# Kernel tuning notes

Measured on AMD Instinct MI355X. Metric: run time of the kernel, lower is better.

## Reference

```python
import jax, jax.numpy as jnp
import numpy as np

B, D, N, M = 64, 128, 400, 50
H, KD = 8, 16
NCONV, K, PAD = 4, 7, 3
MAXTS = 10000.0


def _pe(l):
    # PositionEncoding: freqs/phases interleave sin/cos as sin(pos*f + phase)
    i = np.arange(D)
    freqs = MAXTS ** np.where(i % 2 == 0, -i / D, -(i - 1) / D)
    phases = np.where(i % 2 == 0, 0.0, np.pi / 2)
    pos = np.arange(l)
    return jnp.asarray(np.sin(pos[None, :] * freqs[:, None] + phases[:, None]).astype(np.float32))  # [D, l]


def _ln(x, g, b, eps=1e-6):
    # LayerNorm1d over channel dim of [B, D, L]; torch .std() is unbiased (ddof=1), divides by (std+eps)
    mu = x.mean(axis=1, keepdims=True)
    sd = x.std(axis=1, keepdims=True, ddof=1)
    return g[None, :, None] * (x - mu) / (sd + eps) + b[None, :, None]


def _attn(xT, mask, Wq, bq, Wk, bk, Wv, bv, Wo, bo):
    # xT: [B, L, D]; per-head linears vectorized over the head axis
    q = jnp.einsum('bld,hdk->bhlk', xT, Wq) + bq[None, :, None, :]
    k = jnp.einsum('bld,hdk->bhlk', xT, Wk) + bk[None, :, None, :]
    v = jnp.einsum('bld,hdk->bhlk', xT, Wv) + bv[None, :, None, :]
    sc = jnp.einsum('bhik,bhjk->bhij', q, k) / np.sqrt(KD)
    sc = sc - 1e30 * (1.0 - mask[:, None, None, :])  # mask over key positions
    a = jax.nn.softmax(sc, axis=-1)
    o = jnp.einsum('bhij,bhjk->bhik', a, v)
    o = o.transpose(0, 2, 1, 3).reshape(xT.shape[0], xT.shape[1], H * KD)
    return o @ Wo + bo


def _fwd(context_emb, question_emb, c_mask, q_mask, ln_g, ln_b, dw_w, dw_b, pw_w, pw_b,
         Wq, bq, Wk, bk, Wv, bv, Wo, bo, Wfc, bfc, cq_wc, cq_wq, cq_wm, cq_b):
    def block(x, mask):
        out = x + _pe(x.shape[2])[None]
        for i in range(NCONV):  # fixed small layer loop
            res = out
            h = _ln(out, ln_g, ln_b)
            h = jax.lax.conv_general_dilated(h, dw_w[i], (1,), [(PAD, PAD)],
                                             feature_group_count=D,
                                             dimension_numbers=('NCH', 'OIH', 'NCH')) + dw_b[i][None, :, None]
            h = jnp.einsum('bdl,ed->bel', h, pw_w[i]) + pw_b[i][None, :, None]
            out = jax.nn.relu(h) + res  # eval-mode layer_dropout = inputs + residual
        res = out
        h = _ln(out, ln_g, ln_b)
        h = _attn(h.transpose(0, 2, 1), mask, Wq, bq, Wk, bk, Wv, bv, Wo, bo)
        out = h.transpose(0, 2, 1) + res
        res = out
        h = _ln(out, ln_g, ln_b)
        h = jnp.einsum('bdl,ed->bel', h, Wfc) + bfc[None, :, None]
        return h + res

    C = block(context_emb, c_mask)
    Q = block(question_emb, q_mask)
    C2 = C.transpose(0, 2, 1)  # [B, N, D]
    Q2 = Q.transpose(0, 2, 1)  # [B, M, D]
    # Biaffine similarity W0([Q; C; Q*C]) decomposed (same math, no [B,N*M,3D] materialization)
    S = (C2 @ cq_wc)[:, :, None] + (Q2 @ cq_wq)[:, None, :] \
        + jnp.einsum('bnd,bmd->bnm', C2 * cq_wm, Q2) + cq_b[0]
    S_r = jax.nn.softmax(S - 1e30 * (1.0 - q_mask[:, None, :]), axis=2)
    S_c = jax.nn.softmax(S - 1e30 * (1.0 - c_mask[:, :, None]), axis=1)
    A = S_r @ Q2                                    # context-to-query [B, N, D]
    Bt = jnp.einsum('bnm,bkm->bnk', S_r, S_c) @ C2  # query-to-context (DCN style) [B, N, D]
    return jnp.concatenate([C2, A, C2 * A, C2 * Bt], axis=-1)  # [B, N, 4D]


def setup_inputs() -> dict:
    key = jax.random.key(0)
    ks = jax.random.split(key, 16)
    s = 1.0 / np.sqrt(D)
    return dict(
        context_emb=jax.random.normal(ks[0], (B, D, N), jnp.float32),
        question_emb=jax.random.normal(ks[1], (B, D, M), jnp.float32),
        c_mask=jnp.ones((B, N), jnp.float32),
        q_mask=jnp.ones((B, M), jnp.float32),
        ln_g=jnp.ones((D,), jnp.float32),
        ln_b=jnp.zeros((D,), jnp.float32),
        dw_w=jax.random.normal(ks[2], (NCONV, D, 1, K), jnp.float32) / np.sqrt(K),
        dw_b=jnp.zeros((NCONV, D), jnp.float32),
        pw_w=jax.random.normal(ks[3], (NCONV, D, D), jnp.float32) * s,
        pw_b=jnp.zeros((NCONV, D), jnp.float32),
        Wq=jax.random.normal(ks[4], (H, D, KD), jnp.float32) * s,
        bq=jnp.zeros((H, KD), jnp.float32),
        Wk=jax.random.normal(ks[5], (H, D, KD), jnp.float32) * s,
        bk=jnp.zeros((H, KD), jnp.float32),
        Wv=jax.random.normal(ks[6], (H, D, KD), jnp.float32) * s,
        bv=jnp.zeros((H, KD), jnp.float32),
        Wo=jax.random.normal(ks[7], (H * KD, D), jnp.float32) * s,
        bo=jnp.zeros((D,), jnp.float32),
        Wfc=jax.random.normal(ks[8], (D, D), jnp.float32) * s,
        bfc=jnp.zeros((D,), jnp.float32),
        cq_wc=jax.random.normal(ks[9], (D,), jnp.float32) * s,
        cq_wq=jax.random.normal(ks[10], (D,), jnp.float32) * s,
        cq_wm=jax.random.normal(ks[11], (D,), jnp.float32) * s,
        cq_b=jnp.zeros((1,), jnp.float32),
    )


def reference(context_emb, question_emb, c_mask, q_mask, ln_g, ln_b, dw_w, dw_b, pw_w, pw_b,
              Wq, bq, Wk, bk, Wv, bv, Wo, bo, Wfc, bfc, cq_wc, cq_wq, cq_wm, cq_b):
    return _fwd(context_emb, question_emb, c_mask, q_mask, ln_g, ln_b, dw_w, dw_b, pw_w, pw_b,
                Wq, bq, Wk, bk, Wv, bv, Wo, bo, Wfc, bfc, cq_wc, cq_wq, cq_wm, cq_b)
```

## Files before the change

kernel.cpp:

```cpp
#include <hip/hip_runtime.h>
#include <math.h>

#define BB 64
#define DD 128
#define NN 400
#define MM 50
#define HH 8
#define KDIM 16
#define NC 4
#define KW 7

#define SZ_C (BB * DD * NN)
#define SZ_Q (BB * DD * MM)
#define SSTAT (BB * NN + BB * MM)

__global__ void k_transposeW(const float* __restrict__ pw_w, const float* __restrict__ Wo,
                             const float* __restrict__ Wfc, const float* __restrict__ Wq,
                             const float* __restrict__ Wk, const float* __restrict__ Wv,
                             float* __restrict__ Wcan) {
  int idx = blockIdx.x * 256 + threadIdx.x;
  if (idx >= 9 * 16384) return;
  int m = idx >> 14;
  int r = idx & 16383;
  int d = r >> 7, e = r & 127;
  float v;
  if (m < 4) v = pw_w[m * 16384 + e * 128 + d];
  else if (m == 4) v = Wo[d * 128 + e];
  else if (m == 5) v = Wfc[e * 128 + d];
  else {
    const float* W = (m == 6) ? Wq : (m == 7) ? Wk : Wv;
    v = W[((e >> 4) * 128 + d) * 16 + (e & 15)];
  }
  Wcan[idx] = v;
}

__global__ void k_pestats(const float* __restrict__ xC, const float* __restrict__ xQ,
                          float* __restrict__ yC, float* __restrict__ yQ,
                          float* __restrict__ mu, float* __restrict__ inv) {
  int blk = blockIdx.x;
  const float* x; float* y; int L, l0, b, soff;
  if (blk < 448) { b = blk / 7; l0 = (blk % 7) * 64; x = xC; y = yC; L = NN; soff = 0; }
  else { b = blk - 448; l0 = 0; x = xQ; y = yQ; L = MM; soff = BB * NN; }
  int tid = threadIdx.x;
  int ll = tid & 63;
  int dq = tid >> 6;
  int l = l0 + ll;
  __shared__ float s_sum[4][64], s_sq[4][64];
  float sum = 0.f, sq = 0.f;
  if (l < L) {
    const float* px = x + (size_t)b * DD * L + l;
    float* py = y + (size_t)b * DD * L + l;
    for (int d = dq * 32; d < dq * 32 + 32; ++d) {
      int de = d & ~1;
      float freq = __expf((float)de * (-9.210340371976184f / 128.0f));
      float ph = (d & 1) ? 1.5707963267948966f : 0.0f;
      float v = px[(size_t)d * L] + sinf((float)l * freq + ph);
      py[(size_t)d * L] = v;
      sum += v; sq += v * v;
    }
  }
  s_sum[dq][ll] = sum; s_sq[dq][ll] = sq;
  __syncthreads();
  if (dq == 0 && l < L) {
    float ts = s_sum[0][ll] + s_sum[1][ll] + s_sum[2][ll] + s_sum[3][ll];
    float tq = s_sq[0][ll] + s_sq[1][ll] + s_sq[2][ll] + s_sq[3][ll];
    float m = ts * (1.0f / 128.0f);
    float var = (tq - 128.0f * m * m) * (1.0f / 127.0f);
    float sd = sqrtf(fmaxf(var, 0.f));
    mu[soff + b * L + l] = m;
    inv[soff + b * L + l] = 1.0f / (sd + 1e-6f);
  }
}

__global__ __launch_bounds__(256, 2) void k_convgemm(
    const float* __restrict__ xC, const float* __restrict__ xQ,
    float* __restrict__ outC, float* __restrict__ outQ,
    const float* __restrict__ Wc, const float* __restrict__ pwb,
    const float* __restrict__ dww, const float* __restrict__ dwb,
    const float* __restrict__ muI, const float* __restrict__ invI,
    float* __restrict__ muO, float* __restrict__ invO,
    const float* __restrict__ g, const float* __restrict__ beta) {
  int blk = blockIdx.x;
  int b = blk >> 3, tile = blk & 7;
  const float* x; float* out; int L, l0, soff;
  if (tile < 7) { x = xC; out = outC; L = NN; l0 = tile * 64; soff = 0; }
  else { x = xQ; out = outQ; L = MM; l0 = 0; soff = BB * NN; }
  __shared__ float Wl[32 * 128];
  __shared__ float Xl[32 * 64];
  __shared__ float Sm[70], Si[70];
  int tid = threadIdx.x;
  const float* xb = x + (size_t)b * DD * L;
  for (int t = tid; t < 70; t += 256) {
    int gl = l0 + t - 3;
    bool ok = (gl >= 0 && gl < L);
    Sm[t] = ok ? muI[soff + b * L + gl] : 0.f;
    Si[t] = ok ? invI[soff + b * L + gl] : 0.f;
  }
  float acc[8][4];
  #pragma unroll
  for (int i = 0; i < 8; ++i)
    #pragma unroll
    for (int j = 0; j < 4; ++j) acc[i][j] = 0.f;
  __syncthreads();
  for (int kc = 0; kc < 4; ++kc) {
    int d0 = kc * 32;
    #pragma unroll
    for (int i = 0; i < 4; ++i) {
      int idx = i * 256 + tid;
      ((float4*)Wl)[idx] = ((const float4*)Wc)[(size_t)d0 * 32 + idx];
    }
    #pragma unroll
    for (int r = 0; r < 2; ++r) {
      int k = r * 16 + (tid >> 4);
      int d = d0 + k;
      int c0 = (tid & 15) * 4;
      const float* xrow = xb + (size_t)d * L;
      float gd = g[d], bd = beta[d];
      float wv[7];
      #pragma unroll
      for (int u = 0; u < 7; ++u) wv[u] = dww[d * 7 + u];
      float dbv = dwb[d];
      float xw[10];
      int gbase = l0 + c0 - 3;
      if (gbase >= 1 && gbase + 11 <= L && (((unsigned)(d * L + gbase - 1)) & 3u) == 0u) {
        const float4* p = (const float4*)&xrow[gbase - 1];
        float4 A = p[0], Bv = p[1], Cv = p[2];
        float xr[12] = {A.x, A.y, A.z, A.w, Bv.x, Bv.y, Bv.z, Bv.w, Cv.x, Cv.y, Cv.z, Cv.w};
        #pragma unroll
        for (int s = 0; s < 10; ++s)
          xw[s] = gd * (xr[s + 1] - Sm[c0 + s]) * Si[c0 + s] + bd;
      } else {
        #pragma unroll
        for (int s = 0; s < 10; ++s) {
          int gl = gbase + s;
          float v = 0.f;
          if (gl >= 0 && gl < L)
            v = gd * (xrow[gl] - Sm[c0 + s]) * Si[c0 + s] + bd;
          xw[s] = v;
        }
      }
      float4 o;
      o.x = dbv; o.y = dbv; o.z = dbv; o.w = dbv;
      #pragma unroll
      for (int u = 0; u < 7; ++u) {
        o.x += wv[u] * xw[u];
        o.y += wv[u] * xw[u + 1];
        o.z += wv[u] * xw[u + 2];
        o.w += wv[u] * xw[u + 3];
      }
      *(float4*)&Xl[k * 64 + c0] = o;
    }
    __syncthreads();
    int e0 = (tid >> 4) * 8, cq = (tid & 15) * 4;
    for (int k = 0; k < 32; ++k) {
      const float4* wp = (const float4*)&Wl[k * 128 + e0];
      float4 w0 = wp[0], w1 = wp[1];
      float4 xv = *(const float4*)&Xl[k * 64 + cq];
      float we[8] = {w0.x, w0.y, w0.z, w0.w, w1.x, w1.y, w1.z, w1.w};
      float xe[4] = {xv.x, xv.y, xv.z, xv.w};
      #pragma unroll
      for (int i = 0; i < 8; ++i)
        #pragma unroll
        for (int j = 0; j < 4; ++j) acc[i][j] += we[i] * xe[j];
    }
    __syncthreads();
  }
  int e0 = (tid >> 4) * 8, cq = (tid & 15) * 4;
  float ssum[4], ssq[4];
  #pragma unroll
  for (int j = 0; j < 4; ++j) { ssum[j] = 0.f; ssq[j] = 0.f; }
  #pragma unroll
  for (int i = 0; i < 8; ++i) {
    float bi = pwb[e0 + i];
    float* po = out + ((size_t)b * DD + e0 + i) * L;
    const float* pr = xb + (size_t)(e0 + i) * L;
    #pragma unroll
    for (int j = 0; j < 4; ++j) {
      int l = l0 + cq + j;
      if (l < L) {
        float v = fmaxf(acc[i][j] + bi, 0.f) + pr[l];
        po[l] = v;
        ssum[j] += v; ssq[j] += v * v;
      }
    }
  }
  int grp = tid >> 4;
  #pragma unroll
  for (int j = 0; j < 4; ++j) {
    Xl[grp * 64 + cq + j] = ssum[j];
    Wl[grp * 64 + cq + j] = ssq[j];
  }
  __syncthreads();
  if (tid < 64) {
    int l = l0 + tid;
    if (l < L) {
      float ts = 0.f, tq = 0.f;
      #pragma unroll
      for (int gg = 0; gg < 16; ++gg) { ts += Xl[gg * 64 + tid]; tq += Wl[gg * 64 + tid]; }
      float m = ts * (1.0f / 128.0f);
      float var = (tq - 128.0f * m * m) * (1.0f / 127.0f);
      float sd = sqrtf(fmaxf(var, 0.f));
      muO[soff + b * L + l] = m;
      invO[soff + b * L + l] = 1.0f / (sd + 1e-6f);
    }
  }
}

template <int LNF, int ACT, int STATS, int TRANS>
__global__ __launch_bounds__(256) void k_gemm64(
    const float* __restrict__ xC, const float* __restrict__ xQ,
    float* __restrict__ outC, float* __restrict__ outQ,
    const float* __restrict__ Wc, const float* __restrict__ bias,
    const float* __restrict__ mu, const float* __restrict__ inv,
    float* __restrict__ muO, float* __restrict__ invO,
    const float* __restrict__ g, const float* __restrict__ beta,
    float* __restrict__ C2o, float* __restrict__ Q2o,
    float* __restrict__ cdo, float* __restrict__ qdo,
    const float* __restrict__ wc, const float* __restrict__ wq) {
  int blk = blockIdx.x;
  int b = blk >> 3, tile = blk & 7;
  const float* x; float* out; int L, l0, soff;
  if (tile < 7) { x = xC; out = outC; L = NN; l0 = tile * 64; soff = 0; }
  else { x = xQ; out = outQ; L = MM; l0 = 0; soff = BB * NN; }
  __shared__ float Wl[TRANS ? 64 * 68 : 32 * 128];
  __shared__ float Xl[TRANS ? 64 * 68 : 32 * 64];
  int tid = threadIdx.x;
  float acc[8][4];
  #pragma unroll
  for (int i = 0; i < 8; ++i)
    #pragma unroll
    for (int j = 0; j < 4; ++j) acc[i][j] = 0.f;
  const float* xb = x + (size_t)b * DD * L;
  const float* pmu = mu + soff + b * L;
  const float* pin = inv + soff + b * L;
  for (int kc = 0; kc < 4; ++kc) {
    int d0 = kc * 32;
    #pragma unroll
    for (int i = 0; i < 4; ++i) {
      int idx = i * 256 + tid;
      ((float4*)Wl)[idx] = ((const float4*)Wc)[(size_t)d0 * 32 + idx];
    }
    #pragma unroll
    for (int t = 0; t < 8; ++t) {
      int idx = t * 256 + tid;
      int k = idx >> 6, l = idx & 63;
      float v = 0.f;
      int gl = l0 + l;
      if (gl < L) {
        v = xb[(size_t)(d0 + k) * L + gl];
        if (LNF) v = g[d0 + k] * (v - pmu[gl]) * pin[gl] + beta[d0 + k];
      }
      Xl[idx] = v;
    }
    __syncthreads();
    int e0 = (tid >> 4) * 8, cq = (tid & 15) * 4;
    for (int k = 0; k < 32; ++k) {
      const float4* wp = (const float4*)&Wl[k * 128 + e0];
      float4 w0 = wp[0], w1 = wp[1];
      float4 xv = *(const float4*)&Xl[k * 64 + cq];
      float we[8] = {w0.x, w0.y, w0.z, w0.w, w1.x, w1.y, w1.z, w1.w};
      float xe[4] = {xv.x, xv.y, xv.z, xv.w};
      #pragma unroll
      for (int i = 0; i < 8; ++i)
        #pragma unroll
        for (int j = 0; j < 4; ++j) acc[i][j] += we[i] * xe[j];
    }
    __syncthreads();
  }
  int e0 = (tid >> 4) * 8, cq = (tid & 15) * 4;
  float ssum[4], ssq[4];
  #pragma unroll
  for (int j = 0; j < 4; ++j) { ssum[j] = 0.f; ssq[j] = 0.f; }
  #pragma unroll
  for (int i = 0; i < 8; ++i) {
    float bi = bias[e0 + i];
    float* po = out + ((size_t)b * DD + e0 + i) * L;
    #pragma unroll
    for (int j = 0; j < 4; ++j) {
      int l = l0 + cq + j;
      if (l < L) {
        float v = acc[i][j] + bi;
        if (ACT != 0) v += po[l];
        po[l] = v;
        if (STATS) { ssum[j] += v; ssq[j] += v * v; }
        if (TRANS) {
          float* T = (e0 < 64) ? Wl : Xl;
          T[(cq + j) * 68 + (e0 & 63) + i] = v;
        }
      }
    }
  }
  if (STATS) {
    int grp = tid >> 4;
    #pragma unroll
    for (int j = 0; j < 4; ++j) {
      Xl[grp * 64 + cq + j] = ssum[j];
      Wl[grp * 64 + cq + j] = ssq[j];
    }
    __syncthreads();
    if (tid < 64) {
      int l = l0 + tid;
      if (l < L) {
        float ts = 0.f, tq = 0.f;
        #pragma unroll
        for (int gg = 0; gg < 16; ++gg) { ts += Xl[gg * 64 + tid]; tq += Wl[gg * 64 + tid]; }
        float m = ts * (1.0f / 128.0f);
        float var = (tq - 128.0f * m * m) * (1.0f / 127.0f);
        float sd = sqrtf(fmaxf(var, 0.f));
        muO[soff + b * L + l] = m;
        invO[soff + b * L + l] = 1.0f / (sd + 1e-6f);
      }
    }
  }
  if (TRANS) {
    __syncthreads();
    int r = tid >> 2, seg = tid & 3;
    int gl = l0 + r;
    const float* wsel = (tile < 7) ? wc : wq;
    float* Y2 = (tile < 7) ? C2o : Q2o;
    float* dd = (tile < 7) ? cdo : qdo;
    float part = 0.f;
    if (gl < L) {
      float4* dst = (float4*)(Y2 + ((size_t)b * L + gl) * 128);
      #pragma unroll
      for (int q8 = 0; q8 < 8; ++q8) {
        int e = seg * 32 + q8 * 4;
        const float* T = (e < 64) ? Wl : Xl;
        float4 v4 = *(const float4*)&T[r * 68 + (e & 63)];
        dst[seg * 8 + q8] = v4;
        float4 w4 = *(const float4*)&wsel[e];
        part += v4.x * w4.x + v4.y * w4.y + v4.z * w4.z + v4.w * w4.w;
      }
    }
    part += __shfl_xor(part, 1);
    part += __shfl_xor(part, 2);
    if (gl < L && seg == 0) dd[b * L + gl] = part;
  }
}

__global__ __launch_bounds__(256) void k_gemm_qkv(
    const float* __restrict__ xC, const float* __restrict__ xQ,
    float* __restrict__ o1C, float* __restrict__ o1Q,
    float* __restrict__ o2C, float* __restrict__ o2Q,
    float* __restrict__ o3C, float* __restrict__ o3Q,
    const float* __restrict__ Wcan,
    const float* __restrict__ bq, const float* __restrict__ bk, const float* __restrict__ bv,
    const float* __restrict__ mu, const float* __restrict__ inv,
    const float* __restrict__ g, const float* __restrict__ beta) {
  int blk0 = blockIdx.x;
  int grp = blk0 >> 9;
  int blk = blk0 & 511;
  const float* Wc = Wcan + (size_t)(6 + grp) * 16384;
  const float* bias = (grp == 0) ? bq : (grp == 1) ? bk : bv;
  float* oC = (grp == 0) ? o1C : (grp == 1) ? o2C : o3C;
  float* oQ = (grp == 0) ? o1Q : (grp == 1) ? o2Q : o3Q;
  int b = blk >> 3, tile = blk & 7;
  const float* x; float* out; int L, l0, soff;
  if (tile < 7) { x = xC; out = oC; L = NN; l0 = tile * 64; soff = 0; }
  else { x = xQ; out = oQ; L = MM; l0 = 0; soff = BB * NN; }
  __shared__ float Wl[32 * 128];
  __shared__ float Xl[32 * 64];
  int tid = threadIdx.x;
  float acc[8][4];
  #pragma unroll
  for (int i = 0; i < 8; ++i)
    #pragma unroll
    for (int j = 0; j < 4; ++j) acc[i][j] = 0.f;
  const float* xb = x + (size_t)b * DD * L;
  const float* pmu = mu + soff + b * L;
  const float* pin = inv + soff + b * L;
  for (int kc = 0; kc < 4; ++kc) {
    int d0 = kc * 32;
    #pragma unroll
    for (int i = 0; i < 4; ++i) {
      int idx = i * 256 + tid;
      ((float4*)Wl)[idx] = ((const float4*)Wc)[(size_t)d0 * 32 + idx];
    }
    #pragma unroll
    for (int t = 0; t < 8; ++t) {
      int idx = t * 256 + tid;
      int k = idx >> 6, l = idx & 63;
      float v = 0.f;
      int gl = l0 + l;
      if (gl < L) {
        v = xb[(size_t)(d0 + k) * L + gl];
        v = g[d0 + k] * (v - pmu[gl]) * pin[gl] + beta[d0 + k];
      }
      Xl[idx] = v;
    }
    __syncthreads();
    int e0 = (tid >> 4) * 8, cq = (tid & 15) * 4;
    for (int k = 0; k < 32; ++k) {
      const float4* wp = (const float4*)&Wl[k * 128 + e0];
      float4 w0 = wp[0], w1 = wp[1];
      float4 xv = *(const float4*)&Xl[k * 64 + cq];
      float we[8] = {w0.x, w0.y, w0.z, w0.w, w1.x, w1.y, w1.z, w1.w};
      float xe[4] = {xv.x, xv.y, xv.z, xv.w};
      #pragma unroll
      for (int i = 0; i < 8; ++i)
        #pragma unroll
        for (int j = 0; j < 4; ++j) acc[i][j] += we[i] * xe[j];
    }
    __syncthreads();
  }
  int e0 = (tid >> 4) * 8, cq = (tid & 15) * 4;
  #pragma unroll
  for (int i = 0; i < 8; ++i) {
    float bi = bias[e0 + i];
    float* po = out + ((size_t)b * DD + e0 + i) * L;
    #pragma unroll
    for (int j = 0; j < 4; ++j) {
      int l = l0 + cq + j;
      if (l < L) po[l] = acc[i][j] + bi;
    }
  }
}

__global__ __launch_bounds__(256) void k_attn2(
    const float* __restrict__ qC, const float* __restrict__ kC, const float* __restrict__ vC,
    const float* __restrict__ qQ, const float* __restrict__ kQ, const float* __restrict__ vQ,
    const float* __restrict__ cmask, const float* __restrict__ qmask,
    float* __restrict__ oC, float* __restrict__ oQ) {
  int blk = blockIdx.x;
  const float *qp, *kp, *vp, *mk; float* op; int L, b, h, q0, qcnt;
  if (blk < 1024) {
    b = blk >> 4; h = (blk >> 1) & 7; int half = blk & 1;
    qp = qC; kp = kC; vp = vC; mk = cmask; op = oC; L = NN;
    q0 = half * 256; qcnt = half ? (NN - 256) : 256;
  } else {
    int bb = blk - 1024; b = bb >> 3; h = bb & 7;
    qp = qQ; kp = kQ; vp = vQ; mk = qmask; op = oQ; L = MM;
    q0 = 0; qcnt = MM;
  }
  __shared__ float Kl[NN * KDIM];
  __shared__ float Vl[NN * KDIM];
  __shared__ float Ml[NN];
  int tid = threadIdx.x;
  size_t base = ((size_t)b * DD + h * KDIM) * L;
  int KP = (L + 7) & ~7;
  for (int idx = tid; idx < KDIM * L; idx += 256) {
    int t = idx / L, j = idx - t * L;
    Kl[j * KDIM + t] = kp[base + (size_t)t * L + j];
    Vl[j * KDIM + t] = vp[base + (size_t)t * L + j];
  }
  for (int idx = tid; idx < (KP - L) * KDIM; idx += 256) {
    int j = L + (idx >> 4), t = idx & 15;
    Kl[j * KDIM + t] = 0.f; Vl[j * KDIM + t] = 0.f;
  }
  for (int j = tid; j < KP; j += 256)
    Ml[j] = (j < L) ? -1e30f * (1.0f - mk[b * L + j]) : -1e30f;
  __syncthreads();
  if (tid >= qcnt) return;

  int i = q0 + tid;
  float q[KDIM];
  #pragma unroll
  for (int t = 0; t < KDIM; ++t) q[t] = qp[base + (size_t)t * L + i] * 0.25f;
  float m = -1e30f, ls = 0.f;
  float acc[KDIM];
  #pragma unroll
  for (int t = 0; t < KDIM; ++t) acc[t] = 0.f;
  for (int j0 = 0; j0 < KP; j0 += 8) {
    const float4* mp = (const float4*)&Ml[j0];
    float4 ma0 = mp[0], ma1 = mp[1];
    float mav[8] = {ma0.x, ma0.y, ma0.z, ma0.w, ma1.x, ma1.y, ma1.z, ma1.w};
    float s[8];
    #pragma unroll
    for (int jj = 0; jj < 8; ++jj) {
      const float4* kf = (const float4*)&Kl[(j0 + jj) * KDIM];
      float4 k0 = kf[0], k1 = kf[1], k2 = kf[2], k3 = kf[3];
      float da = q[0] * k0.x + q[1] * k0.y + q[2] * k0.z + q[3] * k0.w
               + q[4] * k1.x + q[5] * k1.y + q[6] * k1.z + q[7] * k1.w;
      float db = q[8] * k2.x + q[9] * k2.y + q[10] * k2.z + q[11] * k2.w
               + q[12] * k3.x + q[13] * k3.y + q[14] * k3.z + q[15] * k3.w;
      s[jj] = da + db + mav[jj];
    }
    float cm = s[0];
    #pragma unroll
    for (int jj = 1; jj < 8; ++jj) cm = fmaxf(cm, s[jj]);
    if (cm > m) {
      float sc = __expf(m - cm);
      ls *= sc;
      #pragma unroll
      for (int t = 0; t < KDIM; ++t) acc[t] *= sc;
      m = cm;
    }
    #pragma unroll
    for (int jj = 0; jj < 8; ++jj) {
      float p = __expf(s[jj] - m);
      ls += p;
      const float4* vf = (const float4*)&Vl[(j0 + jj) * KDIM];
      float4 v0 = vf[0], v1 = vf[1], v2 = vf[2], v3 = vf[3];
      acc[0] += p * v0.x;  acc[1] += p * v0.y;  acc[2] += p * v0.z;  acc[3] += p * v0.w;
      acc[4] += p * v1.x;  acc[5] += p * v1.y;  acc[6] += p * v1.z;  acc[7] += p * v1.w;
      acc[8] += p * v2.x;  acc[9] += p * v2.y;  acc[10] += p * v2.z; acc[11] += p * v2.w;
      acc[12] += p * v3.x; acc[13] += p * v3.y; acc[14] += p * v3.z; acc[15] += p * v3.w;
    }
  }
  float invl = 1.0f / ls;
  #pragma unroll
  for (int t = 0; t < KDIM; ++t)
    op[base + (size_t)t * L + i] = acc[t] * invl;
}

__global__ __launch_bounds__(256) void k_S2(
    const float* __restrict__ C2, const float* __restrict__ Q2,
    const float* __restrict__ cd, const float* __restrict__ qd,
    const float* __restrict__ wm, const float* __restrict__ bias,
    float* __restrict__ S) {
  int blk = blockIdx.x;
  int b = blk / 7, nt = blk % 7;
  int n0 = nt * 64;
  int nv = NN - n0; if (nv > 64) nv = 64;
  __shared__ float Cw[64 * 132];
  __shared__ float Ql[52 * 132];
  __shared__ float cdl[64];
  __shared__ float qdl[50];
  int tid = threadIdx.x;
  const float4* c4g = (const float4*)(C2 + (size_t)b * NN * DD);
  const float4* q4g = (const float4*)(Q2 + (size_t)b * MM * DD);
  const float4* w4 = (const float4*)wm;
  for (int i = tid; i < 64 * 32; i += 256) {
    int n = i >> 5, d4 = i & 31;
    float4 v = {0.f, 0.f, 0.f, 0.f};
    if (n < nv) {
      float4 c = c4g[(size_t)(n0 + n) * 32 + d4];
      float4 w = w4[d4];
      v.x = c.x * w.x; v.y = c.y * w.y; v.z = c.z * w.z; v.w = c.w * w.w;
    }
    *(float4*)&Cw[n * 132 + d4 * 4] = v;
  }
  for (int i = tid; i < 52 * 32; i += 256) {
    int m = i >> 5, d4 = i & 31;
    float4 v = {0.f, 0.f, 0.f, 0.f};
    if (m < MM) v = q4g[(size_t)m * 32 + d4];
    *(float4*)&Ql[m * 132 + d4 * 4] = v;
  }
  if (tid < 64) cdl[tid] = (tid < nv) ? cd[b * NN + n0 + tid] : 0.f;
  if (tid >= 64 && tid < 114) qdl[tid - 64] = qd[b * MM + (tid - 64)];
  __syncthreads();
  int n = tid >> 2, mg = tid & 3;
  int m0 = mg * 13;
  float acc[13];
  #pragma unroll
  for (int k = 0; k < 13; ++k) acc[k] = 0.f;
  const float* cp = &Cw[n * 132];
  for (int d4 = 0; d4 < 32; ++d4) {
    float4 c = *(const float4*)&cp[d4 * 4];
    #pragma unroll
    for (int k = 0; k < 13; ++k) {
      float4 q = *(const float4*)&Ql[(m0 + k) * 132 + d4 * 4];
      acc[k] += c.x * q.x + c.y * q.y + c.z * q.z + c.w * q.w;
    }
  }
  if (n < nv) {
    float add = cdl[n] + bias[0];
    float* ps = S + ((size_t)b * NN + n0 + n) * MM + m0;
    #pragma unroll
    for (int k = 0; k < 13; ++k) {
      int m = m0 + k;
      if (m < MM) ps[k] = acc[k] + add + qdl[m];
    }
  }
}

__global__ void k_smaxU(const float* __restrict__ S, float* __restrict__ Sr,
                        const float* __restrict__ cmask, const float* __restrict__ qmask,
                        const float* __restrict__ C2, float* __restrict__ U) {
  int blk = blockIdx.x;
  int tid = threadIdx.x;
  if (blk < BB * MM) {
    int b = blk / MM;
    int mcol = blk % MM;
    __shared__ float Sl[NN];
    float vals[7];
    float mx = -1e30f;
    #pragma unroll
    for (int c = 0; c < 7; ++c) {
      int n = tid + c * 64;
      float s = -1e30f;
      if (n < NN)
        s = S[((size_t)b * NN + n) * MM + mcol] - 1e30f * (1.0f - cmask[b * NN + n]);
      vals[c] = s;
      mx = fmaxf(mx, s);
    }
    #pragma unroll
    for (int off = 1; off < 64; off <<= 1) mx = fmaxf(mx, __shfl_xor(mx, off));
    float sum = 0.f;
    #pragma unroll
    for (int c = 0; c < 7; ++c) { vals[c] = __expf(vals[c] - mx); sum += vals[c]; }
    #pragma unroll
    for (int off = 1; off < 64; off <<= 1) sum += __shfl_xor(sum, off);
    float inv = 1.0f / sum;
    #pragma unroll
    for (int c = 0; c < 7; ++c) {
      int n = tid + c * 64;
      if (n < NN) Sl[n] = vals[c] * inv;
    }
    __syncthreads();
    const float2* c2 = (const float2*)(C2 + (size_t)b * NN * DD) + tid;
    float2 a = {0.f, 0.f};
    #pragma unroll 4
    for (int kk = 0; kk < NN; ++kk) {
      float s = Sl[kk];
      float2 c = c2[(size_t)kk * 64];
      a.x += s * c.x; a.y += s * c.y;
    }
    ((float2*)(U + ((size_t)b * MM + mcol) * DD))[tid] = a;
  } else {
    int bn = blk - BB * MM;
    int b = bn / NN;
    float s = -1e30f;
    if (tid < MM)
      s = S[(size_t)bn * MM + tid] - 1e30f * (1.0f - qmask[b * MM + tid]);
    float mx = s;
    #pragma unroll
    for (int off = 1; off < 64; off <<= 1) mx = fmaxf(mx, __shfl_xor(mx, off));
    float e = (tid < MM) ? __expf(s - mx) : 0.f;
    float sum = e;
    #pragma unroll
    for (int off = 1; off < 64; off <<= 1) sum += __shfl_xor(sum, off);
    if (tid < MM) Sr[(size_t)bn * MM + tid] = e / sum;
  }
}

__global__ __launch_bounds__(256) void k_ABtF(
    const float* __restrict__ Sr, const float* __restrict__ Q2,
    const float* __restrict__ Uu, const float* __restrict__ C2,
    float* __restrict__ out) {
  int blk = blockIdx.x;
  int b = blk / 7, nt = blk % 7;
  int n0 = nt * 64;
  int nv = NN - n0; if (nv > 64) nv = 64;
  __shared__ float Ql[MM * 128];
  __shared__ float Ul[MM * 128];
  __shared__ float Sl[64 * MM];
  int tid = threadIdx.x;
  const float4* q4 = (const float4*)(Q2 + (size_t)b * MM * DD);
  const float4* u4 = (const float4*)(Uu + (size_t)b * MM * DD);
  for (int i = tid; i < MM * 32; i += 256) {
    ((float4*)Ql)[i] = q4[i];
    ((float4*)Ul)[i] = u4[i];
  }
  for (int i = tid; i < 64 * MM; i += 256) {
    int n = i / MM;
    Sl[i] = (n < nv) ? Sr[((size_t)b * NN + n0 + n) * MM + (i - n * MM)] : 0.f;
  }
  __syncthreads();
  int n = tid >> 2;
  if (n >= nv) return;
  int d04 = (tid & 3) * 8;
  float4 accA[8], accB[8];
  #pragma unroll
  for (int r = 0; r < 8; ++r) {
    accA[r] = {0.f, 0.f, 0.f, 0.f};
    accB[r] = {0.f, 0.f, 0.f, 0.f};
  }
  const float* sp = &Sl[n * MM];
  for (int m = 0; m < MM; ++m) {
    float s = sp[m];
    const float4* qp = (const float4*)&Ql[m * 128] + d04;
    const float4* up = (const float4*)&Ul[m * 128] + d04;
    #pragma unroll
    for (int r = 0; r < 8; ++r) {
      float4 q = qp[r], u = up[r];
      accA[r].x += s * q.x; accA[r].y += s * q.y; accA[r].z += s * q.z; accA[r].w += s * q.w;
      accB[r].x += s * u.x; accB[r].y += s * u.y; accB[r].z += s * u.z; accB[r].w += s * u.w;
    }
  }
  int gn = n0 + n;
  const float4* c4 = (const float4*)(C2 + ((size_t)b * NN + gn) * DD) + d04;
  float4* po = (float4*)(out + (size_t)(b * NN + gn) * 512);
  #pragma unroll
  for (int r = 0; r < 8; ++r) {
    float4 c = c4[r];
    float4 a = accA[r], bt = accB[r];
    po[d04 + r] = c;
    po[32 + d04 + r] = a;
    float4 ca = {c.x * a.x, c.y * a.y, c.z * a.z, c.w * a.w};
    po[64 + d04 + r] = ca;
    float4 cb = {c.x * bt.x, c.y * bt.y, c.z * bt.z, c.w * bt.w};
    po[96 + d04 + r] = cb;
  }
}

extern "C" void kernel_launch(void* const* d_in, const int* in_sizes, int n_in,
                              void* d_out, int out_size, void* d_ws, size_t ws_size,
                              hipStream_t stream) {
  (void)in_sizes; (void)n_in; (void)out_size; (void)ws_size;
  const float* ctx   = (const float*)d_in[0];
  const float* que   = (const float*)d_in[1];
  const float* cmask = (const float*)d_in[2];
  const float* qmask = (const float*)d_in[3];
  const float* ln_g  = (const float*)d_in[4];
  const float* ln_b  = (const float*)d_in[5];
  const float* dw_w  = (const float*)d_in[6];
  const float* dw_b  = (const float*)d_in[7];
  const float* pw_w  = (const float*)d_in[8];
  const float* pw_b  = (const float*)d_in[9];
  const float* Wq    = (const float*)d_in[10];
  const float* bq    = (const float*)d_in[11];
  const float* Wk    = (const float*)d_in[12];
  const float* bk    = (const float*)d_in[13];
  const float* Wv    = (const float*)d_in[14];
  const float* bv    = (const float*)d_in[15];
  const float* Wo    = (const float*)d_in[16];
  const float* bo    = (const float*)d_in[17];
  const float* Wfc   = (const float*)d_in[18];
  const float* bfc   = (const float*)d_in[19];
  const float* cq_wc = (const float*)d_in[20];
  const float* cq_wq = (const float*)d_in[21];
  const float* cq_wm = (const float*)d_in[22];
  const float* cq_b  = (const float*)d_in[23];
  float* out = (float*)d_out;
  float* ws = (float*)d_ws;

  float* Cb   = ws;
  float* Qb   = Cb + SZ_C;
  float* t1C  = Qb + SZ_Q;
  float* t1Q  = t1C + SZ_C;
  float* t2C  = t1Q + SZ_Q;
  float* t2Q  = t2C + SZ_C;
  float* t3C  = t2Q + SZ_Q;
  float* t3Q  = t3C + SZ_C;
  float* t4C  = t3Q + SZ_Q;
  float* t4Q  = t4C + SZ_C;
  float* mu0  = t4Q + SZ_Q;
  float* inv0 = mu0 + SSTAT;
  float* mu1  = inv0 + SSTAT;
  float* inv1 = mu1 + SSTAT;
  float* Wcan = inv1 + SSTAT;

  k_transposeW<<<(9 * 16384 + 255) / 256, 256, 0, stream>>>(pw_w, Wo, Wfc, Wq, Wk, Wv, Wcan);
  k_pestats<<<512, 256, 0, stream>>>(ctx, que, Cb, Qb, mu0, inv0);

  for (int i = 0; i < NC; ++i) {
    const float* inC = (i & 1) ? t1C : Cb;
    const float* inQ = (i & 1) ? t1Q : Qb;
    float* oC = (i & 1) ? Cb : t1C;
    float* oQ = (i & 1) ? Qb : t1Q;
    const float* mI = (i & 1) ? mu1 : mu0;
    const float* iI = (i & 1) ? inv1 : inv0;
    float* mO = (i & 1) ? mu0 : mu1;
    float* iO = (i & 1) ? inv0 : inv1;
    k_convgemm<<<512, 256, 0, stream>>>(inC, inQ, oC, oQ,
                                        Wcan + (size_t)i * 16384, pw_b + (size_t)i * DD,
                                        dw_w + (size_t)i * DD * KW, dw_b + (size_t)i * DD,
                                        mI, iI, mO, iO, ln_g, ln_b);
  }
  k_gemm_qkv<<<1536, 256, 0, stream>>>(Cb, Qb, t1C, t1Q, t2C, t2Q, t3C, t3Q,
                                       Wcan, bq, bk, bv, mu0, inv0, ln_g, ln_b);
  k_attn2<<<1536, 256, 0, stream>>>(t1C, t2C, t3C, t1Q, t2Q, t3Q, cmask, qmask, t4C, t4Q);

  float* C2  = t1C;
  float* Q2  = t1Q;
  float* S   = t2C;
  float* Sr  = t2C + 1638400;
  float* Uu  = t2Q;
  float* cd  = t3Q;
  float* qd  = t4Q + SZ_Q - BB * MM;

  k_gemm64<0, 1, 1, 0><<<512, 256, 0, stream>>>(t4C, t4Q, Cb, Qb, Wcan + 4 * 16384, bo,
                                                mu0, inv0, mu1, inv1, ln_g, ln_b,
                                                nullptr, nullptr, nullptr, nullptr,
                                                nullptr, nullptr);
  k_gemm64<1, 1, 0, 1><<<512, 256, 0, stream>>>(Cb, Qb, Cb, Qb, Wcan + 5 * 16384, bfc,
                                                mu1, inv1, mu0, inv0, ln_g, ln_b,
                                                C2, Q2, cd, qd, cq_wc, cq_wq);

  k_S2<<<448, 256, 0, stream>>>(C2, Q2, cd, qd, cq_wm, cq_b, S);
  k_smaxU<<<BB * MM + BB * NN, 64, 0, stream>>>(S, Sr, cmask, qmask, C2, Uu);
  k_ABtF<<<448, 256, 0, stream>>>(Sr, Q2, Uu, C2, out);
}
```

Before: 621.0 us.

## Fuse row softmax into similarity kernel and vectorize full-tile GEMM input loads

```diff
diff --git a/kernel.cpp b/kernel.cpp
--- a/kernel.cpp
+++ b/kernel.cpp
@@ -233,6 +233,7 @@
   const float* xb = x + (size_t)b * DD * L;
   const float* pmu = mu + soff + b * L;
   const float* pin = inv + soff + b * L;
+  bool fullt = (l0 + 63 < L);
   for (int kc = 0; kc < 4; ++kc) {
     int d0 = kc * 32;
     #pragma unroll
@@ -240,17 +241,37 @@
       int idx = i * 256 + tid;
       ((float4*)Wl)[idx] = ((const float4*)Wc)[(size_t)d0 * 32 + idx];
     }
-    #pragma unroll
-    for (int t = 0; t < 8; ++t) {
-      int idx = t * 256 + tid;
-      int k = idx >> 6, l = idx & 63;
-      float v = 0.f;
-      int gl = l0 + l;
-      if (gl < L) {
-        v = xb[(size_t)(d0 + k) * L + gl];
-        if (LNF) v = g[d0 + k] * (v - pmu[gl]) * pin[gl] + beta[d0 + k];
-      }
-      Xl[idx] = v;
+    if (fullt) {
+      #pragma unroll
+      for (int t = 0; t < 2; ++t) {
+        int idx = t * 256 + tid;
+        int k = idx >> 4, c4 = (idx & 15) * 4;
+        int gl = l0 + c4;
+        float4 v = *(const float4*)&xb[(size_t)(d0 + k) * L + gl];
+        if (LNF) {
+          float4 m4 = *(const float4*)&pmu[gl];
+          float4 i4 = *(const float4*)&pin[gl];
+          float gk = g[d0 + k], bk = beta[d0 + k];
+          v.x = gk * (v.x - m4.x) * i4.x + bk;
+          v.y = gk * (v.y - m4.y) * i4.y + bk;
+          v.z = gk * (v.z - m4.z) * i4.z + bk;
+          v.w = gk * (v.w - m4.w) * i4.w + bk;
+        }
+        *(float4*)&Xl[k * 64 + c4] = v;
+      }
+    } else {
+      #pragma unroll
+      for (int t = 0; t < 8; ++t) {
+        int idx = t * 256 + tid;
+        int k = idx >> 6, l = idx & 63;
+        float v = 0.f;
+        int gl = l0 + l;
+        if (gl < L) {
+          v = xb[(size_t)(d0 + k) * L + gl];
+          if (LNF) v = g[d0 + k] * (v - pmu[gl]) * pin[gl] + beta[d0 + k];
+        }
+        Xl[idx] = v;
+      }
     }
     __syncthreads();
     int e0 = (tid >> 4) * 8, cq = (tid & 15) * 4;
@@ -369,6 +390,7 @@
   const float* xb = x + (size_t)b * DD * L;
   const float* pmu = mu + soff + b * L;
   const float* pin = inv + soff + b * L;
+  bool fullt = (l0 + 63 < L);
   for (int kc = 0; kc < 4; ++kc) {
     int d0 = kc * 32;
     #pragma unroll
@@ -376,17 +398,35 @@
       int idx = i * 256 + tid;
       ((float4*)Wl)[idx] = ((const float4*)Wc)[(size_t)d0 * 32 + idx];
     }
-    #pragma unroll
-    for (int t = 0; t < 8; ++t) {
-      int idx = t * 256 + tid;
-      int k = idx >> 6, l = idx & 63;
-      float v = 0.f;
-      int gl = l0 + l;
-      if (gl < L) {
-        v = xb[(size_t)(d0 + k) * L + gl];
-        v = g[d0 + k] * (v - pmu[gl]) * pin[gl] + beta[d0 + k];
-      }
-      Xl[idx] = v;
+    if (fullt) {
+      #pragma unroll
+      for (int t = 0; t < 2; ++t) {
+        int idx = t * 256 + tid;
+        int k = idx >> 4, c4 = (idx & 15) * 4;
+        int gl = l0 + c4;
+        float4 v = *(const float4*)&xb[(size_t)(d0 + k) * L + gl];
+        float4 m4 = *(const float4*)&pmu[gl];
+        float4 i4 = *(const float4*)&pin[gl];
+        float gk = g[d0 + k], bk = beta[d0 + k];
+        v.x = gk * (v.x - m4.x) * i4.x + bk;
+        v.y = gk * (v.y - m4.y) * i4.y + bk;
+        v.z = gk * (v.z - m4.z) * i4.z + bk;
+        v.w = gk * (v.w - m4.w) * i4.w + bk;
+        *(float4*)&Xl[k * 64 + c4] = v;
+      }
+    } else {
+      #pragma unroll
+      for (int t = 0; t < 8; ++t) {
+        int idx = t * 256 + tid;
+        int k = idx >> 6, l = idx & 63;
+        float v = 0.f;
+        int gl = l0 + l;
+        if (gl < L) {
+          v = xb[(size_t)(d0 + k) * L + gl];
+          v = g[d0 + k] * (v - pmu[gl]) * pin[gl] + beta[d0 + k];
+        }
+        Xl[idx] = v;
+      }
     }
     __syncthreads();
     int e0 = (tid >> 4) * 8, cq = (tid & 15) * 4;
@@ -507,7 +547,8 @@
     const float* __restrict__ C2, const float* __restrict__ Q2,
     const float* __restrict__ cd, const float* __restrict__ qd,
     const float* __restrict__ wm, const float* __restrict__ bias,
-    float* __restrict__ S) {
+    const float* __restrict__ qmask,
+    float* __restrict__ S, float* __restrict__ Sr) {
   int blk = blockIdx.x;
   int b = blk / 7, nt = blk % 7;
   int n0 = nt * 64;
@@ -516,6 +557,7 @@
   __shared__ float Ql[52 * 132];
   __shared__ float cdl[64];
   __shared__ float qdl[50];
+  __shared__ float qml[52];
   int tid = threadIdx.x;
   const float4* c4g = (const float4*)(C2 + (size_t)b * NN * DD);
   const float4* q4g = (const float4*)(Q2 + (size_t)b * MM * DD);
@@ -538,6 +580,10 @@
   }
   if (tid < 64) cdl[tid] = (tid < nv) ? cd[b * NN + n0 + tid] : 0.f;
   if (tid >= 64 && tid < 114) qdl[tid - 64] = qd[b * MM + (tid - 64)];
+  if (tid >= 114 && tid < 166) {
+    int m = tid - 114;
+    qml[m] = (m < MM) ? -1e30f * (1.0f - qmask[b * MM + m]) : -1e30f;
+  }
   __syncthreads();
   int n = tid >> 2, mg = tid & 3;
   int m0 = mg * 13;
@@ -553,75 +599,85 @@
       acc[k] += c.x * q.x + c.y * q.y + c.z * q.z + c.w * q.w;
     }
   }
+  float add = (n < nv) ? (cdl[n] + bias[0]) : 0.f;
+  float mx = -1e30f;
+  #pragma unroll
+  for (int k = 0; k < 13; ++k) {
+    int m = m0 + k;
+    acc[k] += add + ((m < MM) ? qdl[m] : 0.f);
+    float sm = acc[k] + qml[m];
+    mx = fmaxf(mx, sm);
+  }
+  mx = fmaxf(mx, __shfl_xor(mx, 1));
+  mx = fmaxf(mx, __shfl_xor(mx, 2));
+  float ex[13];
+  float sum = 0.f;
+  #pragma unroll
+  for (int k = 0; k < 13; ++k) {
+    int m = m0 + k;
+    float e = __expf(acc[k] + qml[m] - mx);
+    if (m >= MM) e = 0.f;
+    ex[k] = e;
+    sum += e;
+  }
+  sum += __shfl_xor(sum, 1);
+  sum += __shfl_xor(sum, 2);
   if (n < nv) {
-    float add = cdl[n] + bias[0];
+    float inv = 1.0f / sum;
     float* ps = S + ((size_t)b * NN + n0 + n) * MM + m0;
+    float* pr = Sr + ((size_t)b * NN + n0 + n) * MM + m0;
     #pragma unroll
     for (int k = 0; k < 13; ++k) {
       int m = m0 + k;
-      if (m < MM) ps[k] = acc[k] + add + qdl[m];
-    }
-  }
-}
-
-__global__ void k_smaxU(const float* __restrict__ S, float* __restrict__ Sr,
-                        const float* __restrict__ cmask, const float* __restrict__ qmask,
-                        const float* __restrict__ C2, float* __restrict__ U) {
+      if (m < MM) {
+        ps[k] = acc[k];
+        pr[k] = ex[k] * inv;
+      }
+    }
+  }
+}
+
+__global__ void k_smaxUcol(const float* __restrict__ S, const float* __restrict__ cmask,
+                           const float* __restrict__ C2, float* __restrict__ U) {
   int blk = blockIdx.x;
   int tid = threadIdx.x;
-  if (blk < BB * MM) {
-    int b = blk / MM;
-    int mcol = blk % MM;
-    __shared__ float Sl[NN];
-    float vals[7];
-    float mx = -1e30f;
-    #pragma unroll
-    for (int c = 0; c < 7; ++c) {
-      int n = tid + c * 64;
-      float s = -1e30f;
-      if (n < NN)
-        s = S[((size_t)b * NN + n) * MM + mcol] - 1e30f * (1.0f - cmask[b * NN + n]);
-      vals[c] = s;
-      mx = fmaxf(mx, s);
-    }
-    #pragma unroll
-    for (int off = 1; off < 64; off <<= 1) mx = fmaxf(mx, __shfl_xor(mx, off));
-    float sum = 0.f;
-    #pragma unroll
-    for (int c = 0; c < 7; ++c) { vals[c] = __expf(vals[c] - mx); sum += vals[c]; }
-    #pragma unroll
-    for (int off = 1; off < 64; off <<= 1) sum += __shfl_xor(sum, off);
-    float inv = 1.0f / sum;
-    #pragma unroll
-    for (int c = 0; c < 7; ++c) {
-      int n = tid + c * 64;
-      if (n < NN) Sl[n] = vals[c] * inv;
-    }
-    __syncthreads();
-    const float2* c2 = (const float2*)(C2 + (size_t)b * NN * DD) + tid;
-    float2 a = {0.f, 0.f};
-    #pragma unroll 4
-    for (int kk = 0; kk < NN; ++kk) {
-      float s = Sl[kk];
-      float2 c = c2[(size_t)kk * 64];
-      a.x += s * c.x; a.y += s * c.y;
-    }
-    ((float2*)(U + ((size_t)b * MM + mcol) * DD))[tid] = a;
-  } else {
-    int bn = blk - BB * MM;
-    int b = bn / NN;
+  int b = blk / MM;
+  int mcol = blk % MM;
+  __shared__ float Sl[NN];
+  float vals[7];
+  float mx = -1e30f;
+  #pragma unroll
+  for (int c = 0; c < 7; ++c) {
+    int n = tid + c * 64;
     float s = -1e30f;
-    if (tid < MM)
-      s = S[(size_t)bn * MM + tid] - 1e30f * (1.0f - qmask[b * MM + tid]);
-    float mx = s;
-    #pragma unroll
-    for (int off = 1; off < 64; off <<= 1) mx = fmaxf(mx, __shfl_xor(mx, off));
-    float e = (tid < MM) ? __expf(s - mx) : 0.f;
-    float sum = e;
-    #pragma unroll
-    for (int off = 1; off < 64; off <<= 1) sum += __shfl_xor(sum, off);
-    if (tid < MM) Sr[(size_t)bn * MM + tid] = e / sum;
-  }
+    if (n < NN)
+      s = S[((size_t)b * NN + n) * MM + mcol] - 1e30f * (1.0f - cmask[b * NN + n]);
+    vals[c] = s;
+    mx = fmaxf(mx, s);
+  }
+  #pragma unroll
+  for (int off = 1; off < 64; off <<= 1) mx = fmaxf(mx, __shfl_xor(mx, off));
+  float sum = 0.f;
+  #pragma unroll
+  for (int c = 0; c < 7; ++c) { vals[c] = __expf(vals[c] - mx); sum += vals[c]; }
+  #pragma unroll
+  for (int off = 1; off < 64; off <<= 1) sum += __shfl_xor(sum, off);
+  float inv = 1.0f / sum;
+  #pragma unroll
+  for (int c = 0; c < 7; ++c) {
+    int n = tid + c * 64;
+    if (n < NN) Sl[n] = vals[c] * inv;
+  }
+  __syncthreads();
+  const float2* c2 = (const float2*)(C2 + (size_t)b * NN * DD) + tid;
+  float2 a = {0.f, 0.f};
+  #pragma unroll 4
+  for (int kk = 0; kk < NN; ++kk) {
+    float s = Sl[kk];
+    float2 c = c2[(size_t)kk * 64];
+    a.x += s * c.x; a.y += s * c.y;
+  }
+  ((float2*)(U + ((size_t)b * MM + mcol) * DD))[tid] = a;
 }
 
 __global__ __launch_bounds__(256) void k_ABtF(
@@ -768,7 +824,7 @@
                                                 mu1, inv1, mu0, inv0, ln_g, ln_b,
                                                 C2, Q2, cd, qd, cq_wc, cq_wq);
 
-  k_S2<<<448, 256, 0, stream>>>(C2, Q2, cd, qd, cq_wm, cq_b, S);
-  k_smaxU<<<BB * MM + BB * NN, 64, 0, stream>>>(S, Sr, cmask, qmask, C2, Uu);
+  k_S2<<<448, 256, 0, stream>>>(C2, Q2, cd, qd, cq_wm, cq_b, qmask, S, Sr);
+  k_smaxUcol<<<BB * MM, 64, 0, stream>>>(S, cmask, C2, Uu);
   k_ABtF<<<448, 256, 0, stream>>>(Sr, Q2, Uu, C2, out);
 }
```

Result: no change. 625.3 us (+0.7%).
